# Kernel optimization log

Hardware: AMD Instinct MI355X
Metric: run time of the kernel (lower is better)

## Reference

```python
import jax, jax.numpy as jnp
import numpy as np

D = 2048; N_H = 16; D_H = 128; D_R = 64; FFN = 8192
THETA = 1000000.0; EPS = 1e-6
SCALE = 1.0 / np.sqrt(D_H + D_R)


def rms_norm(x, w):
    xf = x.astype(jnp.float32)
    n = jax.lax.rsqrt(jnp.mean(xf * xf, axis=-1, keepdims=True) + EPS)
    return (xf * n).astype(x.dtype) * w


def build_rope_cache(seq_len, dim):
    freqs = 1.0 / (THETA ** (jnp.arange(0, dim, 2, dtype=jnp.float32) / dim))
    f = jnp.arange(seq_len, dtype=jnp.float32)[:, None] * freqs[None, :]  # (S, dim/2)
    cos = jnp.repeat(jnp.cos(f), 2, axis=-1)  # (S, dim)
    sin = jnp.repeat(jnp.sin(f), 2, axis=-1)
    return cos, sin


def apply_rope(x, cos, sin):
    # x: (B, H, S, d); cos/sin: (S, d)
    x1 = x[..., ::2]
    x2 = x[..., 1::2]
    x_rot = jnp.stack([-x2, x1], axis=-1).reshape(x.shape)
    return x * cos + x_rot * sin


def setup_inputs() -> dict:
    key = jax.random.key(0)
    ks = jax.random.split(key, 16)
    B, M, N = 2, 2048, 2048
    s = 0.02
    return {
        "query": jax.random.normal(ks[0], (B, M, D), jnp.float32),
        "key_value": jax.random.normal(ks[1], (B, N, D), jnp.float32),
        "g_q": jnp.ones((D,), jnp.float32),
        "g_kv": jnp.ones((D,), jnp.float32),
        "g_ffn": jnp.ones((D,), jnp.float32),
        "w_qc": jax.random.normal(ks[2], (D, N_H * D_H), jnp.float32) * s,
        "w_kc": jax.random.normal(ks[3], (D, N_H * D_H), jnp.float32) * s,
        "w_qr": jax.random.normal(ks[4], (D, N_H * D_R), jnp.float32) * s,
        "w_kr": jax.random.normal(ks[5], (D, N_H * D_R), jnp.float32) * s,
        "w_v": jax.random.normal(ks[6], (D, N_H * D_H), jnp.float32) * s,
        "w_o": jax.random.normal(ks[7], (N_H * D_H, D), jnp.float32) * s,
        "w_gate": jax.random.normal(ks[8], (D, FFN), jnp.float32) * s,
        "w_up": jax.random.normal(ks[9], (D, FFN), jnp.float32) * s,
        "w_down": jax.random.normal(ks[10], (FFN, D), jnp.float32) * s,
    }


def reference(query, key_value, g_q, g_kv, g_ffn, w_qc, w_kc, w_qr, w_kr, w_v, w_o, w_gate, w_up, w_down):
    B, M, _ = query.shape
    N = key_value.shape[1]

    qn = rms_norm(query, g_q)
    kvn = rms_norm(key_value, g_kv)

    Q_C = (qn @ w_qc).reshape(B, M, N_H, D_H).transpose(0, 2, 1, 3)   # bhmd
    K_C = (kvn @ w_kc).reshape(B, N, N_H, D_H).transpose(0, 2, 1, 3)  # bhnd
    Q_R = (qn @ w_qr).reshape(B, M, N_H, D_R).transpose(0, 2, 1, 3)
    K_R = (kvn @ w_kr).reshape(B, N, N_H, D_R).transpose(0, 2, 1, 3)
    V = (kvn @ w_v).reshape(B, N, N_H, D_H).transpose(0, 2, 1, 3)

    cos, sin = build_rope_cache(max(M, N), D_R)
    Q_R = apply_rope(Q_R, cos[:M], sin[:M])
    K_R = apply_rope(K_R, cos[:N], sin[:N])

    scores = (jnp.einsum('bhmd,bhnd->bhmn', Q_C, K_C)
              + jnp.einsum('bhmr,bhnr->bhmn', Q_R, K_R)) * SCALE
    attn = jax.nn.softmax(scores, axis=-1)
    out = jnp.einsum('bhmn,bhnd->bhmd', attn, V)
    out = out.transpose(0, 2, 1, 3).reshape(B, M, N_H * D_H)
    attn_out = out @ w_o

    x = query + attn_out
    xn = rms_norm(x, g_ffn)
    ffn_out = (jax.nn.silu(xn @ w_gate) * (xn @ w_up)) @ w_down
    return x + ffn_out
```

## Files before the change

kernel.cpp:

```cpp
#include <hip/hip_runtime.h>
#include <stdint.h>


typedef unsigned short u16;
typedef __bf16 bf16x8 __attribute__((ext_vector_type(8)));
typedef unsigned short u16x8 __attribute__((ext_vector_type(8)));
typedef unsigned short u16x4 __attribute__((ext_vector_type(4)));
typedef float f32x4 __attribute__((ext_vector_type(4)));

#define LOG2E 1.4426950408889634f
#define SCALE_F 0.07216878364870323f

__device__ __forceinline__ f32x4 mfma16(bf16x8 a, bf16x8 b, f32x4 c) {
  return __builtin_amdgcn_mfma_f32_16x16x32_bf16(a, b, c, 0, 0, 0);
}

__device__ __forceinline__ u16 f2bf(float f) {
  union { float f; unsigned u; } x; x.f = f;
  unsigned r = x.u + 0x7fffu + ((x.u >> 16) & 1u);
  return (u16)(r >> 16);
}
__device__ __forceinline__ float bf2f(u16 v) {
  union { unsigned u; float f; } x; x.u = ((unsigned)v) << 16;
  return x.f;
}
__device__ __forceinline__ unsigned cvt_pk_bf16(float lo, float hi) {
  unsigned r;
  asm("v_cvt_pk_bf16_f32 %0, %1, %2" : "=v"(r) : "v"(lo), "v"(hi));
  return r;
}

__device__ __forceinline__ void gload_lds16(const u16* g, u16* l) {
  __builtin_amdgcn_global_load_lds(
      (const __attribute__((address_space(1))) unsigned int*)g,
      (__attribute__((address_space(3))) unsigned int*)l, 16, 0, 0);
}

__global__ __launch_bounds__(256) void rmsnorm_k(const float* __restrict__ x,
                                                 const float* __restrict__ g,
                                                 u16* __restrict__ out) {
  const int row = blockIdx.x;
  const int t = threadIdx.x;
  const float* xr = x + (size_t)row * 2048;
  float4 a = ((const float4*)xr)[t * 2];
  float4 b = ((const float4*)xr)[t * 2 + 1];
  float ss = a.x*a.x + a.y*a.y + a.z*a.z + a.w*a.w
           + b.x*b.x + b.y*b.y + b.z*b.z + b.w*b.w;
  #pragma unroll
  for (int off = 32; off; off >>= 1) ss += __shfl_xor(ss, off, 64);
  __shared__ float w4[4];
  if ((t & 63) == 0) w4[t >> 6] = ss;
  __syncthreads();
  ss = w4[0] + w4[1] + w4[2] + w4[3];
  const float n = rsqrtf(ss * (1.0f / 2048.0f) + 1e-6f);
  const float* gr = g + t * 8;
  u16x8 o;
  o[0] = f2bf(a.x * n * gr[0]); o[1] = f2bf(a.y * n * gr[1]);
  o[2] = f2bf(a.z * n * gr[2]); o[3] = f2bf(a.w * n * gr[3]);
  o[4] = f2bf(b.x * n * gr[4]); o[5] = f2bf(b.y * n * gr[5]);
  o[6] = f2bf(b.z * n * gr[6]); o[7] = f2bf(b.w * n * gr[7]);
  *(u16x8*)&out[(size_t)row * 2048 + t * 8] = o;
}

__global__ __launch_bounds__(256) void conv_t(const float* __restrict__ in,
                                              u16* __restrict__ out,
                                              int R, int C, int ldin) {
  __shared__ float tile[64][65];
  const int r0 = blockIdx.y * 64, c0 = blockIdx.x * 64;
  const int tr = threadIdx.x >> 6, tc = threadIdx.x & 63;
  #pragma unroll
  for (int i = 0; i < 16; ++i) {
    int rr = tr * 16 + i;
    tile[rr][tc] = in[(size_t)(r0 + rr) * ldin + c0 + tc];
  }
  __syncthreads();
  #pragma unroll
  for (int i = 0; i < 16; ++i) {
    int rr = tr * 16 + i;
    out[(size_t)(c0 + rr) * R + r0 + tc] = f2bf(tile[tc][rr]);
  }
}

__global__ __launch_bounds__(256) void transpose_bf16(const u16* __restrict__ in,
                                                      u16* __restrict__ out,
                                                      int R, int C) {
  __shared__ u16 tile[64][65];
  const size_t zoff = (size_t)blockIdx.z * R * C;
  const u16* inz = in + zoff;
  u16* outz = out + zoff;
  const int r0 = blockIdx.y * 64, c0 = blockIdx.x * 64;
  const int tr = threadIdx.x >> 6, tc = threadIdx.x & 63;
  #pragma unroll
  for (int i = 0; i < 16; ++i) {
    int rr = tr * 16 + i;
    tile[rr][tc] = inz[(size_t)(r0 + rr) * C + c0 + tc];
  }
  __syncthreads();
  #pragma unroll
  for (int i = 0; i < 16; ++i) {
    int rr = tr * 16 + i;
    outz[(size_t)(c0 + rr) * R + r0 + tc] = tile[tc][rr];
  }
}

__global__ __launch_bounds__(256) void rope_k(u16* __restrict__ buf) {
  const int idx = blockIdx.x * 256 + threadIdx.x;
  const int i = idx & 31;
  const int pos = (idx >> 5) & 2047;
  const int bh = idx >> 16;
  u16* p = buf + ((size_t)(bh * 2048 + pos)) * 192 + 128 + 2 * i;
  const float inv = exp2f(-(float)(2 * i) * (19.931568569324174f / 64.0f));
  const float f = (float)pos * inv;
  const float c = cosf(f), s = sinf(f);
  const float x1 = bf2f(p[0]), x2 = bf2f(p[1]);
  p[0] = f2bf(x1 * c - x2 * s);
  p[1] = f2bf(x2 * c + x1 * s);
}

template <int EPI>
__global__ __launch_bounds__(256) void gemm_bt(const u16* __restrict__ A,
                                               const u16* __restrict__ Bt,
                                               int N, int K,
                                               void* __restrict__ outp,
                                               const void* __restrict__ auxp) {
  __shared__ __attribute__((aligned(16))) u16 As[128 * 64];
  __shared__ __attribute__((aligned(16))) u16 Bs[128 * 64];
  const int t = threadIdx.x;
  const int wv = t >> 6, quad = (t >> 4) & 3, ln = t & 15;

  const int nbx = gridDim.x;
  const int lin = blockIdx.y * nbx + blockIdx.x;
  const int cpx = (nbx * gridDim.y) >> 3;
  const int swz = (lin & 7) * cpx + (lin >> 3);
  const int bm0 = (swz / nbx) * 128, bn0 = (swz % nbx) * 128;
  const int wm = (wv >> 1) * 64, wn = (wv & 1) * 64;

  f32x4 acc[4][4] = {};

  int srow[4], scol[4];
  #pragma unroll
  for (int i = 0; i < 4; ++i) {
    const int row = i * 32 + (t >> 3);
    const int cB = ((t & 7) * 16) ^ ((row & 7) << 4);
    srow[i] = row;
    scol[i] = cB >> 1;
  }

  for (int kk = 0; kk < K; kk += 64) {
    #pragma unroll
    for (int i = 0; i < 4; ++i) {
      gload_lds16(&A[(size_t)(bm0 + srow[i]) * K + kk + scol[i]],
                  &As[i * 2048 + t * 8]);
      gload_lds16(&Bt[(size_t)(bn0 + srow[i]) * K + kk + scol[i]],
                  &Bs[i * 2048 + t * 8]);
    }
    __syncthreads();
    #pragma unroll
    for (int ks = 0; ks < 2; ++ks) {
      bf16x8 af[4], bfr[4];
      #pragma unroll
      for (int mt = 0; mt < 4; ++mt) {
        const int row = wm + mt * 16 + ln;
        af[mt] = *(const bf16x8*)&As[row * 64 +
                   (((ks * 64 + quad * 16) ^ ((row & 7) << 4)) >> 1)];
      }
      #pragma unroll
      for (int nt = 0; nt < 4; ++nt) {
        const int row = wn + nt * 16 + ln;
        bfr[nt] = *(const bf16x8*)&Bs[row * 64 +
                   (((ks * 64 + quad * 16) ^ ((row & 7) << 4)) >> 1)];
      }
      #pragma unroll
      for (int mt = 0; mt < 4; ++mt)
        #pragma unroll
        for (int nt = 0; nt < 4; ++nt)
          acc[mt][nt] = mfma16(af[mt], bfr[nt], acc[mt][nt]);
    }
    __syncthreads();
  }

  #pragma unroll
  for (int mt = 0; mt < 4; ++mt) {
    #pragma unroll
    for (int r = 0; r < 4; ++r) {
      const int gm = bm0 + wm + mt * 16 + quad * 4 + r;
      #pragma unroll
      for (int nt = 0; nt < 4; ++nt) {
        const int gn = bn0 + wn + nt * 16 + ln;
        float v = acc[mt][nt][r];
        if constexpr (EPI == 0) {
          ((u16*)outp)[(size_t)gm * N + gn] = f2bf(v);
        } else if constexpr (EPI >= 1 && EPI <= 4) {
          if constexpr (EPI == 1 || EPI == 2) v *= SCALE_F * LOG2E;
          const int bb = gm >> 11, mm = gm & 2047;
          int h, d, off;
          if constexpr (EPI == 1 || EPI == 3) { h = gn >> 7; d = gn & 127; off = 0; }
          else                                { h = gn >> 6; d = gn & 63; off = 128; }
          ((u16*)outp)[((size_t)((bb * 16 + h) * 2048 + mm)) * 192 + off + d] = f2bf(v);
        } else if constexpr (EPI == 5) {
          const int bb = gm >> 11, mm = gm & 2047;
          const int h = gn >> 7, d = gn & 127;
          ((u16*)outp)[((size_t)((bb * 16 + h) * 2048 + mm)) * 128 + d] = f2bf(v);
        } else if constexpr (EPI == 6) {
          ((float*)outp)[(size_t)gm * N + gn] =
              v + ((const float*)auxp)[(size_t)gm * N + gn];
        } else if constexpr (EPI == 7) {
          const float g = bf2f(((const u16*)auxp)[(size_t)gm * N + gn]);
          const float s = g / (1.0f + __expf(-g));
          ((u16*)outp)[(size_t)gm * N + gn] = f2bf(s * v);
        }
      }
    }
  }
}

__global__ __launch_bounds__(256, 2) void flash_k(const u16* __restrict__ Q,
                                                  const u16* __restrict__ K,
                                                  const u16* __restrict__ VT,
                                                  u16* __restrict__ O) {
  __shared__ __attribute__((aligned(16))) u16 Ks[2][64 * 192];
  __shared__ __attribute__((aligned(16))) u16 Vs[128 * 64];

  const int t = threadIdx.x;
  const int wv = t >> 6, quad = (t >> 4) & 3, ln = t & 15;
  const int lane = t & 63;
  const int b = blockIdx.z, h = blockIdx.y;
  const int m0 = blockIdx.x * 128;
  const size_t qbase = ((size_t)(b * 16 + h)) * 2048;
  const u16* kg = K + qbase * 192;
  const u16* vg = VT + ((size_t)(b * 16 + h)) * 128 * 2048;

  int krow[6], kscol[6];
  #pragma unroll
  for (int i = 0; i < 6; ++i) {
    const int o = (wv * 6 + i) * 1024 + lane * 16;
    const int r = o / 384;
    const int c = o - r * 384;
    krow[i] = r;
    kscol[i] = c ^ ((r & 7) << 4);
  }
  int vrow[4], vscol[4];
  #pragma unroll
  for (int i = 0; i < 4; ++i) {
    const int o = (wv * 4 + i) * 1024 + lane * 16;
    const int r = o >> 7;
    vrow[i] = r;
    vscol[i] = (o & 127) ^ ((r & 7) << 4);
  }

  bf16x8 qfA[6], qfB[6];
  {
    const u16* qpA = Q + (qbase + m0 + wv * 16 + ln) * 192 + quad * 8;
    const u16* qpB = qpA + 64 * 192;
    #pragma unroll
    for (int ks = 0; ks < 6; ++ks) {
      qfA[ks] = *(const bf16x8*)&qpA[ks * 32];
      qfB[ks] = *(const bf16x8*)&qpB[ks * 32];
    }
  }

  float mA = -1e30f, lA = 0.0f, mB = -1e30f, lB = 0.0f;
  f32x4 ofA[8] = {}, ofB[8] = {};

  #pragma unroll
  for (int i = 0; i < 6; ++i)
    gload_lds16(kg + (size_t)krow[i] * 192 + (kscol[i] >> 1),
                &Ks[0][(wv * 6 + i) * 512 + lane * 8]);
  #pragma unroll
  for (int i = 0; i < 4; ++i)
    gload_lds16(vg + (size_t)vrow[i] * 2048 + (vscol[i] >> 1),
                &Vs[(wv * 4 + i) * 512 + lane * 8]);
  __syncthreads();

  int cur = 0;
  for (int j = 0; j < 32; ++j) {
    if (j < 31) {
      #pragma unroll
      for (int i = 0; i < 6; ++i)
        gload_lds16(kg + (size_t)((j + 1) * 64 + krow[i]) * 192 + (kscol[i] >> 1),
                    &Ks[cur ^ 1][(wv * 6 + i) * 512 + lane * 8]);
    }

    f32x4 sA[4], sB[4];
    #pragma unroll
    for (int nt = 0; nt < 4; ++nt) {
      f32x4 za = {0.f, 0.f, 0.f, 0.f}, zb = {0.f, 0.f, 0.f, 0.f};
      const int row = nt * 16 + ln;
      const u16* kr = &Ks[cur][row * 192];
      const int sw = (row & 7) << 4;
      #pragma unroll
      for (int ks = 0; ks < 6; ++ks) {
        bf16x8 kb = *(const bf16x8*)&kr[((ks * 64 + quad * 16) ^ sw) >> 1];
        za = mfma16(kb, qfA[ks], za);
        zb = mfma16(kb, qfB[ks], zb);
      }
      sA[nt] = za; sB[nt] = zb;
    }

    float mxA = sA[0][0], mxB = sB[0][0];
    #pragma unroll
    for (int nt = 0; nt < 4; ++nt)
      #pragma unroll
      for (int r = 0; r < 4; ++r) {
        mxA = fmaxf(mxA, sA[nt][r]);
        mxB = fmaxf(mxB, sB[nt][r]);
      }
    mxA = fmaxf(mxA, __shfl_xor(mxA, 16, 64));
    mxA = fmaxf(mxA, __shfl_xor(mxA, 32, 64));
    mxB = fmaxf(mxB, __shfl_xor(mxB, 16, 64));
    mxB = fmaxf(mxB, __shfl_xor(mxB, 32, 64));

    if (__any((mxA > mA + 11.0f) || (mxB > mB + 11.0f))) {
      const float mnA = fmaxf(mA, mxA), mnB = fmaxf(mB, mxB);
      const float aA = exp2f(mA - mnA), aB = exp2f(mB - mnB);
      mA = mnA; mB = mnB;
      lA *= aA; lB *= aB;
      #pragma unroll
      for (int dt = 0; dt < 8; ++dt)
        #pragma unroll
        for (int r = 0; r < 4; ++r) {
          ofA[dt][r] *= aA;
          ofB[dt][r] *= aB;
        }
    }

    float rsA = 0.0f, rsB = 0.0f;
    #pragma unroll
    for (int nt = 0; nt < 4; ++nt)
      #pragma unroll
      for (int r = 0; r < 4; ++r) {
        const float pa = exp2f(sA[nt][r] - mA);
        const float pb = exp2f(sB[nt][r] - mB);
        sA[nt][r] = pa; sB[nt][r] = pb;
        rsA += pa; rsB += pb;
      }
    rsA += __shfl_xor(rsA, 16, 64);
    rsA += __shfl_xor(rsA, 32, 64);
    rsB += __shfl_xor(rsB, 16, 64);
    rsB += __shfl_xor(rsB, 32, 64);
    lA += rsA; lB += rsB;

    unsigned pkA[4][2], pkB[4][2];
    #pragma unroll
    for (int nt = 0; nt < 4; ++nt) {
      pkA[nt][0] = cvt_pk_bf16(sA[nt][0], sA[nt][1]);
      pkA[nt][1] = cvt_pk_bf16(sA[nt][2], sA[nt][3]);
      pkB[nt][0] = cvt_pk_bf16(sB[nt][0], sB[nt][1]);
      pkB[nt][1] = cvt_pk_bf16(sB[nt][2], sB[nt][3]);
    }
    unsigned pawA[2][4], pawB[2][4];
    #pragma unroll
    for (int kt = 0; kt < 2; ++kt)
      #pragma unroll
      for (int w = 0; w < 4; ++w) {
        const int src = ((quad & 1) * 2 + (w >> 1)) * 16 + ln;
        const int loA = __shfl((int)pkA[2 * kt][w & 1], src, 64);
        const int hiA = __shfl((int)pkA[2 * kt + 1][w & 1], src, 64);
        pawA[kt][w] = (unsigned)((quad & 2) ? hiA : loA);
        const int loB = __shfl((int)pkB[2 * kt][w & 1], src, 64);
        const int hiB = __shfl((int)pkB[2 * kt + 1][w & 1], src, 64);
        pawB[kt][w] = (unsigned)((quad & 2) ? hiB : loB);
      }

    __syncthreads();

    #pragma unroll
    for (int kt = 0; kt < 2; ++kt) {
      union { unsigned u[4]; bf16x8 b; } paA, paB;
      #pragma unroll
      for (int w = 0; w < 4; ++w) { paA.u[w] = pawA[kt][w]; paB.u[w] = pawB[kt][w]; }
      #pragma unroll
      for (int dt = 0; dt < 8; ++dt) {
        const int row = dt * 16 + ln;
        const int sw = (row & 7) << 4;
        bf16x8 vb = *(const bf16x8*)&Vs[row * 64 +
                                        (((kt * 64 + quad * 16) ^ sw) >> 1)];
        ofA[dt] = mfma16(vb, paA.b, ofA[dt]);
        ofB[dt] = mfma16(vb, paB.b, ofB[dt]);
      }
    }

    __syncthreads();

    if (j < 31) {
      #pragma unroll
      for (int i = 0; i < 4; ++i)
        gload_lds16(vg + (size_t)vrow[i] * 2048 + (j + 1) * 64 + (vscol[i] >> 1),
                    &Vs[(wv * 4 + i) * 512 + lane * 8]);
    }
    cur ^= 1;
  }

  const float invA = 1.0f / lA, invB = 1.0f / lB;
  #pragma unroll
  for (int dt = 0; dt < 8; ++dt) {
    u16x4 oa, ob;
    #pragma unroll
    for (int r = 0; r < 4; ++r) {
      oa[r] = f2bf(ofA[dt][r] * invA);
      ob[r] = f2bf(ofB[dt][r] * invB);
    }
    *(u16x4*)&O[((size_t)(b * 2048 + m0 + wv * 16 + ln)) * 2048 +
                h * 128 + dt * 16 + quad * 4] = oa;
    *(u16x4*)&O[((size_t)(b * 2048 + m0 + 64 + wv * 16 + ln)) * 2048 +
                h * 128 + dt * 16 + quad * 4] = ob;
  }
}

extern "C" void kernel_launch(void* const* d_in, const int* in_sizes, int n_in,
                              void* d_out, int out_size, void* d_ws, size_t ws_size,
                              hipStream_t stream) {
  const float* query     = (const float*)d_in[0];
  const float* key_value = (const float*)d_in[1];
  const float* g_q       = (const float*)d_in[2];
  const float* g_kv      = (const float*)d_in[3];
  const float* g_ffn     = (const float*)d_in[4];
  const float* w_qc      = (const float*)d_in[5];
  const float* w_kc      = (const float*)d_in[6];
  const float* w_qr      = (const float*)d_in[7];
  const float* w_kr      = (const float*)d_in[8];
  const float* w_v       = (const float*)d_in[9];
  const float* w_o       = (const float*)d_in[10];
  const float* w_gate    = (const float*)d_in[11];
  const float* w_up      = (const float*)d_in[12];
  const float* w_down    = (const float*)d_in[13];

  char* ws = (char*)d_ws;
  const size_t MiB = 1048576;
  u16*   qn   = (u16*)(ws + 0 * MiB);
  u16*   kvn  = (u16*)(ws + 16 * MiB);
  u16*   Qb   = (u16*)(ws + 32 * MiB);
  u16*   Kb   = (u16*)(ws + 56 * MiB);
  u16*   Vb   = (u16*)(ws + 80 * MiB);
  u16*   wt   = (u16*)(ws + 96 * MiB);
  u16*   VT   = (u16*)(ws + 0 * MiB);
  u16*   attn = (u16*)(ws + 16 * MiB);
  float* x    = (float*)(ws + 64 * MiB);
  u16*   xn   = (u16*)(ws + 0 * MiB);
  u16*   ghalf= (u16*)(ws + 16 * MiB);
  u16*   wtf  = (u16*)(ws + 48 * MiB);

  const dim3 blk(256);

  rmsnorm_k<<<4096, blk, 0, stream>>>(query, g_q, qn);
  rmsnorm_k<<<4096, blk, 0, stream>>>(key_value, g_kv, kvn);

  conv_t<<<dim3(32, 32), blk, 0, stream>>>(w_qc, wt, 2048, 2048, 2048);
  gemm_bt<1><<<dim3(16, 32), blk, 0, stream>>>(qn, wt, 2048, 2048, Qb, nullptr);
  conv_t<<<dim3(16, 32), blk, 0, stream>>>(w_qr, wt, 2048, 1024, 1024);
  gemm_bt<2><<<dim3(8, 32), blk, 0, stream>>>(qn, wt, 1024, 2048, Qb, nullptr);
  conv_t<<<dim3(32, 32), blk, 0, stream>>>(w_kc, wt, 2048, 2048, 2048);
  gemm_bt<3><<<dim3(16, 32), blk, 0, stream>>>(kvn, wt, 2048, 2048, Kb, nullptr);
  conv_t<<<dim3(16, 32), blk, 0, stream>>>(w_kr, wt, 2048, 1024, 1024);
  gemm_bt<4><<<dim3(8, 32), blk, 0, stream>>>(kvn, wt, 1024, 2048, Kb, nullptr);
  conv_t<<<dim3(32, 32), blk, 0, stream>>>(w_v, wt, 2048, 2048, 2048);
  gemm_bt<5><<<dim3(16, 32), blk, 0, stream>>>(kvn, wt, 2048, 2048, Vb, nullptr);

  rope_k<<<8192, blk, 0, stream>>>(Qb);
  rope_k<<<8192, blk, 0, stream>>>(Kb);

  transpose_bf16<<<dim3(2, 32, 32), blk, 0, stream>>>(Vb, VT, 2048, 128);

  flash_k<<<dim3(16, 16, 2), blk, 0, stream>>>(Qb, Kb, VT, attn);

  conv_t<<<dim3(32, 32), blk, 0, stream>>>(w_o, wt, 2048, 2048, 2048);
  gemm_bt<6><<<dim3(16, 32), blk, 0, stream>>>(attn, wt, 2048, 2048, x, query);

  rmsnorm_k<<<4096, blk, 0, stream>>>(x, g_ffn, xn);
  for (int h = 0; h < 2; ++h) {
    const int n0 = h * 4096;
    conv_t<<<dim3(64, 32), blk, 0, stream>>>(w_gate + n0, wtf, 2048, 4096, 8192);
    gemm_bt<0><<<dim3(32, 32), blk, 0, stream>>>(xn, wtf, 4096, 2048, ghalf, nullptr);
    conv_t<<<dim3(64, 32), blk, 0, stream>>>(w_up + n0, wtf, 2048, 4096, 8192);
    gemm_bt<7><<<dim3(32, 32), blk, 0, stream>>>(xn, wtf, 4096, 2048, ghalf, ghalf);
    conv_t<<<dim3(32, 64), blk, 0, stream>>>(w_down + (size_t)n0 * 2048, wtf,
                                             4096, 2048, 2048);
    gemm_bt<6><<<dim3(16, 32), blk, 0, stream>>>(ghalf, wtf, 2048, 4096,
                                                 (float*)d_out,
                                                 h == 0 ? (const void*)x
                                                        : (const void*)d_out);
  }
}
```

Baseline: 1.330 ms.

## Add 256x256-tile 512-thread GEMM for FFN gate and up projections

```diff
diff --git a/kernel.cpp b/kernel.cpp
--- a/kernel.cpp
+++ b/kernel.cpp
@@ -34,6 +34,12 @@
   __builtin_amdgcn_global_load_lds(
       (const __attribute__((address_space(1))) unsigned int*)g,
       (__attribute__((address_space(3))) unsigned int*)l, 16, 0, 0);
+}
+
+__device__ __forceinline__ void sbar() {
+  __builtin_amdgcn_sched_barrier(0);
+  __builtin_amdgcn_s_barrier();
+  __builtin_amdgcn_sched_barrier(0);
 }
 
 __global__ __launch_bounds__(256) void rmsnorm_k(const float* __restrict__ x,
@@ -214,6 +220,170 @@
   }
 }
 
+template <int EPI>
+__global__ __launch_bounds__(512, 2) void gemm256(const u16* __restrict__ A,
+                                                  const u16* __restrict__ Bt,
+                                                  int N, int K,
+                                                  void* __restrict__ outp,
+                                                  const void* __restrict__ auxp) {
+  __shared__ __attribute__((aligned(16))) u16 As[2][2][128 * 64];
+  __shared__ __attribute__((aligned(16))) u16 Bs[2][2][128 * 64];
+  const int t = threadIdx.x;
+  const int wv = t >> 6, quad = (t >> 4) & 3, ln = t & 15;
+  const int wm = wv >> 2, wn = wv & 3;
+
+  const int nbx = gridDim.x;
+  const int lin = blockIdx.y * nbx + blockIdx.x;
+  const int cpx = (nbx * gridDim.y) >> 3;
+  const int swz = (lin & 7) * cpx + (lin >> 3);
+  const int bm0 = (swz / nbx) * 256, bn0 = (swz % nbx) * 256;
+
+  f32x4 acc[8][4] = {};
+
+  int srow[2], scol[2];
+  #pragma unroll
+  for (int i = 0; i < 2; ++i) {
+    const int o = i * 8192 + t * 16;
+    const int r = o >> 7;
+    srow[i] = r;
+    scol[i] = ((o & 127) ^ ((r & 7) << 4)) >> 1;
+  }
+
+  #pragma unroll
+  for (int hf = 0; hf < 2; ++hf)
+    #pragma unroll
+    for (int i = 0; i < 2; ++i)
+      gload_lds16(&A[(size_t)(bm0 + hf * 128 + srow[i]) * K + scol[i]],
+                  &As[0][hf][i * 4096 + t * 8]);
+  #pragma unroll
+  for (int hf = 0; hf < 2; ++hf)
+    #pragma unroll
+    for (int i = 0; i < 2; ++i)
+      gload_lds16(&Bt[(size_t)(bn0 + hf * 128 + srow[i]) * K + scol[i]],
+                  &Bs[0][hf][i * 4096 + t * 8]);
+  asm volatile("s_waitcnt vmcnt(0)" ::: "memory");
+  sbar();
+
+  const int NT = K >> 6;
+  for (int kt = 0; kt < NT; ++kt) {
+    const int bsel = kt & 1;
+    const u16* A0 = As[bsel][0];
+    const u16* A1 = As[bsel][1];
+    const u16* B0 = Bs[bsel][0];
+    const u16* B1 = Bs[bsel][1];
+    const bool pf = (kt + 1 < NT);
+    const int knext = (kt + 1) * 64;
+
+    bf16x8 af[2][4], bfr[2][4];
+
+    if (pf) {
+      #pragma unroll
+      for (int hf = 0; hf < 2; ++hf)
+        #pragma unroll
+        for (int i = 0; i < 2; ++i)
+          gload_lds16(&A[(size_t)(bm0 + hf * 128 + srow[i]) * K + knext + scol[i]],
+                      &As[bsel ^ 1][hf][i * 4096 + t * 8]);
+    }
+    #pragma unroll
+    for (int mt = 0; mt < 4; ++mt) {
+      const int row = wm * 64 + mt * 16 + ln;
+      const int sw = (row & 7) << 4;
+      #pragma unroll
+      for (int ks = 0; ks < 2; ++ks)
+        af[ks][mt] = *(const bf16x8*)&A0[row * 64 +
+                       (((ks * 64 + quad * 16) ^ sw) >> 1)];
+    }
+    #pragma unroll
+    for (int nt = 0; nt < 2; ++nt) {
+      const int row = wn * 32 + nt * 16 + ln;
+      const int sw = (row & 7) << 4;
+      #pragma unroll
+      for (int ks = 0; ks < 2; ++ks)
+        bfr[ks][nt] = *(const bf16x8*)&B0[row * 64 +
+                        (((ks * 64 + quad * 16) ^ sw) >> 1)];
+    }
+    __builtin_amdgcn_s_setprio(1);
+    #pragma unroll
+    for (int mt = 0; mt < 4; ++mt)
+      #pragma unroll
+      for (int nt = 0; nt < 2; ++nt)
+        #pragma unroll
+        for (int ks = 0; ks < 2; ++ks)
+          acc[mt][nt] = mfma16(af[ks][mt], bfr[ks][nt], acc[mt][nt]);
+    __builtin_amdgcn_s_setprio(0);
+    sbar();
+
+    if (pf) {
+      #pragma unroll
+      for (int hf = 0; hf < 2; ++hf)
+        #pragma unroll
+        for (int i = 0; i < 2; ++i)
+          gload_lds16(&Bt[(size_t)(bn0 + hf * 128 + srow[i]) * K + knext + scol[i]],
+                      &Bs[bsel ^ 1][hf][i * 4096 + t * 8]);
+    }
+    #pragma unroll
+    for (int nt = 2; nt < 4; ++nt) {
+      const int row = wn * 32 + (nt & 1) * 16 + ln;
+      const int sw = (row & 7) << 4;
+      #pragma unroll
+      for (int ks = 0; ks < 2; ++ks)
+        bfr[ks][nt] = *(const bf16x8*)&B1[row * 64 +
+                        (((ks * 64 + quad * 16) ^ sw) >> 1)];
+    }
+    __builtin_amdgcn_s_setprio(1);
+    #pragma unroll
+    for (int mt = 0; mt < 4; ++mt)
+      #pragma unroll
+      for (int nt = 2; nt < 4; ++nt)
+        #pragma unroll
+        for (int ks = 0; ks < 2; ++ks)
+          acc[mt][nt] = mfma16(af[ks][mt], bfr[ks][nt], acc[mt][nt]);
+    __builtin_amdgcn_s_setprio(0);
+    sbar();
+
+    #pragma unroll
+    for (int mt = 0; mt < 4; ++mt) {
+      const int row = wm * 64 + mt * 16 + ln;
+      const int sw = (row & 7) << 4;
+      #pragma unroll
+      for (int ks = 0; ks < 2; ++ks)
+        af[ks][mt] = *(const bf16x8*)&A1[row * 64 +
+                       (((ks * 64 + quad * 16) ^ sw) >> 1)];
+    }
+    __builtin_amdgcn_s_setprio(1);
+    #pragma unroll
+    for (int mt = 0; mt < 4; ++mt)
+      #pragma unroll
+      for (int nt = 0; nt < 4; ++nt)
+        #pragma unroll
+        for (int ks = 0; ks < 2; ++ks)
+          acc[mt + 4][nt] = mfma16(af[ks][mt], bfr[ks][nt], acc[mt + 4][nt]);
+    __builtin_amdgcn_s_setprio(0);
+    if (pf) asm volatile("s_waitcnt vmcnt(0)" ::: "memory");
+    sbar();
+  }
+
+  #pragma unroll
+  for (int mt = 0; mt < 8; ++mt) {
+    #pragma unroll
+    for (int r = 0; r < 4; ++r) {
+      const int gm = bm0 + (mt >> 2) * 128 + wm * 64 + (mt & 3) * 16 + quad * 4 + r;
+      #pragma unroll
+      for (int nt = 0; nt < 4; ++nt) {
+        const int gn = bn0 + (nt >> 1) * 128 + wn * 32 + (nt & 1) * 16 + ln;
+        float v = acc[mt][nt][r];
+        if constexpr (EPI == 0) {
+          ((u16*)outp)[(size_t)gm * N + gn] = f2bf(v);
+        } else if constexpr (EPI == 7) {
+          const float g = bf2f(((const u16*)auxp)[(size_t)gm * N + gn]);
+          const float s = g / (1.0f + __expf(-g));
+          ((u16*)outp)[(size_t)gm * N + gn] = f2bf(s * v);
+        }
+      }
+    }
+  }
+}
+
 __global__ __launch_bounds__(256, 2) void flash_k(const u16* __restrict__ Q,
                                                   const u16* __restrict__ K,
                                                   const u16* __restrict__ VT,
@@ -470,9 +640,9 @@
   for (int h = 0; h < 2; ++h) {
     const int n0 = h * 4096;
     conv_t<<<dim3(64, 32), blk, 0, stream>>>(w_gate + n0, wtf, 2048, 4096, 8192);
-    gemm_bt<0><<<dim3(32, 32), blk, 0, stream>>>(xn, wtf, 4096, 2048, ghalf, nullptr);
+    gemm256<0><<<dim3(16, 16), dim3(512), 0, stream>>>(xn, wtf, 4096, 2048, ghalf, nullptr);
     conv_t<<<dim3(64, 32), blk, 0, stream>>>(w_up + n0, wtf, 2048, 4096, 8192);
-    gemm_bt<7><<<dim3(32, 32), blk, 0, stream>>>(xn, wtf, 4096, 2048, ghalf, ghalf);
+    gemm256<7><<<dim3(16, 16), dim3(512), 0, stream>>>(xn, wtf, 4096, 2048, ghalf, ghalf);
     conv_t<<<dim3(32, 64), blk, 0, stream>>>(w_down + (size_t)n0 * 2048, wtf,
                                              4096, 2048, 2048);
     gemm_bt<6><<<dim3(16, 32), blk, 0, stream>>>(ghalf, wtf, 2048, 4096,
```

Measured after the change: 1.258 ms. -5.4%, faster.
